# Optimization experiments

Hardware: AMD Instinct MI355X
Metric: run time of the kernel (lower is better)

Reference implementation:

```python
import jax, jax.numpy as jnp
import numpy as np


def setup_inputs() -> dict:
    key = jax.random.key(0)
    ks = jax.random.split(key, 9)
    B, L, D, H, E = 8, 2048, 1024, 256, 8
    Hg = D // 4
    s = 0.02
    return {
        "x": jax.random.normal(ks[0], (B, L, D), dtype=jnp.float32),
        "wg1": jax.random.normal(ks[1], (D, Hg), dtype=jnp.float32) * s,
        "bg1": jax.random.normal(ks[2], (Hg,), dtype=jnp.float32) * s,
        "wg2": jax.random.normal(ks[3], (Hg, E), dtype=jnp.float32) * s,
        "bg2": jax.random.normal(ks[4], (E,), dtype=jnp.float32) * s,
        "w1": jax.random.normal(ks[5], (E, D, H), dtype=jnp.float32) * (1.0 / np.sqrt(D)),
        "b1": jax.random.normal(ks[6], (E, H), dtype=jnp.float32) * s,
        "w2": jax.random.normal(ks[7], (E, H, D), dtype=jnp.float32) * (1.0 / np.sqrt(H)),
        "b2": jax.random.normal(ks[8], (E, D), dtype=jnp.float32) * s,
        "k": 2,
    }


def reference(x, wg1, bg1, wg2, bg2, w1, b1, w2, b2, k):
    B, L, D = x.shape
    xt = x.reshape(-1, D)                       # [T, D] tokens
    T = xt.shape[0]
    # gating MLP: Linear -> GELU(exact, matches torch nn.GELU) -> Linear -> softmax
    logits = jax.nn.gelu(xt @ wg1 + bg1, approximate=False) @ wg2 + bg2  # [T, E]
    scores = jax.nn.softmax(logits, axis=-1)
    top_v, top_i = jax.lax.top_k(scores, k)     # [T, k]
    # dense gate matrix (equivalent to compute_gating's scatter); zeros for non-top-k
    gates = jnp.zeros_like(scores).at[jnp.arange(T)[:, None], top_i].set(top_v)  # [T, E]

    # grouped-GEMM MoE: y[t] = sum_e gates[t,e] * (gelu(x[t] @ W1_e + b1_e) @ W2_e + b2_e)
    # scan over the fixed, small expert axis; gates zero out non-selected experts,
    # giving math identical to the sort/dispatch + per-expert torch.mm loop.
    def body(acc, we):
        w1e, b1e, w2e, b2e, ge = we
        h = jax.nn.gelu(xt @ w1e + b1e, approximate=False)  # [T, H]
        o = h @ w2e + b2e                                    # [T, D]
        return acc + ge[:, None] * o, None

    y, _ = jax.lax.scan(body, jnp.zeros_like(xt), (w1, b1, w2, b2, gates.T))
    return y.reshape(B, L, D)
```

## Files before the change

kernel.cpp:

```cpp
#include <hip/hip_runtime.h>

typedef unsigned short u16;
typedef __attribute__((ext_vector_type(8))) short bf16x8;
typedef __attribute__((ext_vector_type(4))) float f32x4;
typedef __attribute__((ext_vector_type(4))) u16 u16x4;

#define T_TOK 16384
#define D_DIM 1024
#define NE 8
#define MAXP 33792

__device__ __forceinline__ u16 f2bf(float f) {
  union { float f; unsigned int u; } c; c.f = f;
  unsigned int u = c.u;
  u += 0x7fffu + ((u >> 16) & 1u);
  return (u16)(u >> 16);
}

__device__ __forceinline__ float bf2f(u16 v) {
  union { unsigned int u; float f; } c; c.u = ((unsigned int)v) << 16;
  return c.f;
}

__device__ __forceinline__ float gelu_exact(float u) {
  return 0.5f * u * (1.0f + erff(u * 0.70710678118654752f));
}

__device__ __forceinline__ void gld16(const void* g, void* l) {
  __builtin_amdgcn_global_load_lds(
      (const __attribute__((address_space(1))) unsigned int*)g,
      (__attribute__((address_space(3))) unsigned int*)l, 16, 0, 0);
}

__device__ __forceinline__ void stage_tile(u16* lds, const char* g0, size_t stride,
                                           int wid, int lane) {
  const char* g = g0 + (size_t)(wid * 8 + (lane >> 3)) * stride + (size_t)((lane & 7) * 16);
  char* l = (char*)lds + wid * 1024;
  #pragma unroll
  for (int c = 0; c < 4; ++c)
    gld16(g + (size_t)(32 * c) * stride, l + c * 4096);
}

__device__ __forceinline__ void stage_b64x32(u16* lds, const u16* mat, int rowbase,
                                             int k0, int wid, int lane) {
  const int row = wid * 16 + (lane >> 2);
  const char* g = (const char*)(mat + (size_t)(rowbase + row) * 1024 + k0 + (lane & 3) * 8);
  char* l = (char*)lds + wid * 1024;
  gld16(g, l);
}

__device__ __forceinline__ void stage_b32(u16* lds, const u16* mat, int rowbase,
                                          int k0, int wid, int lane) {
  const char* g0 = (const char*)(mat + (size_t)rowbase * 1024 + k0);
  #pragma unroll
  for (int c = 0; c < 2; ++c) {
    const int row = c * 64 + wid * 16 + (lane >> 2);
    const char* g = g0 + (size_t)row * 2048 + (size_t)((lane & 3) * 16);
    char* l = (char*)lds + c * 4096 + wid * 1024;
    gld16(g, l);
  }
}

__device__ __forceinline__ void mma_step(const u16* As, const u16* Bs, f32x4 acc[4][4],
                                         int wm, int wn, int lane) {
  const int r = lane & 15, kq = (lane >> 4) * 8;
  #pragma unroll
  for (int ks = 0; ks < 2; ++ks) {
    const int col = ks * 32 + kq;
    bf16x8 a[4], b[4];
    #pragma unroll
    for (int mf = 0; mf < 4; ++mf)
      a[mf] = *(const bf16x8*)&As[(wm * 64 + mf * 16 + r) * 64 + col];
    #pragma unroll
    for (int nf = 0; nf < 4; ++nf)
      b[nf] = *(const bf16x8*)&Bs[(wn * 64 + nf * 16 + r) * 64 + col];
    #pragma unroll
    for (int mf = 0; mf < 4; ++mf)
      #pragma unroll
      for (int nf = 0; nf < 4; ++nf)
        acc[mf][nf] = __builtin_amdgcn_mfma_f32_16x16x32_bf16(a[mf], b[nf], acc[mf][nf], 0, 0, 0);
  }
}

__global__ __launch_bounds__(256) void cvt_hilo_x_kernel(const float* __restrict__ x,
                                                         u16* __restrict__ xh,
                                                         u16* __restrict__ xl) {
  const int i = (blockIdx.x * 256 + threadIdx.x) * 4;
  float4 v = *(const float4*)(x + i);
  float vv[4] = {v.x, v.y, v.z, v.w};
  u16x4 h, l;
  u16 hh[4], ll[4];
  #pragma unroll
  for (int q = 0; q < 4; ++q) { hh[q] = f2bf(vv[q]); ll[q] = f2bf(vv[q] - bf2f(hh[q])); }
  h.x = hh[0]; h.y = hh[1]; h.z = hh[2]; h.w = hh[3];
  l.x = ll[0]; l.y = ll[1]; l.z = ll[2]; l.w = ll[3];
  *(u16x4*)(xh + i) = h;
  *(u16x4*)(xl + i) = l;
}

__global__ __launch_bounds__(256) void transpose_cvt_kernel(const float* __restrict__ in,
                                                            u16* __restrict__ out,
                                                            int R, int C) {
  __shared__ u16 t[32][36];
  const int e = blockIdx.z;
  const int r0 = blockIdx.x * 32, c0 = blockIdx.y * 32;
  const int tid = threadIdx.x;
  {
    const int r = tid >> 3, cq = (tid & 7) * 4;
    float4 v = *(const float4*)(in + ((size_t)e * R + r0 + r) * C + c0 + cq);
    t[r][cq + 0] = f2bf(v.x); t[r][cq + 1] = f2bf(v.y);
    t[r][cq + 2] = f2bf(v.z); t[r][cq + 3] = f2bf(v.w);
  }
  __syncthreads();
  {
    const int c = tid >> 3, rq = (tid & 7) * 4;
    u16x4 o;
    o.x = t[rq + 0][c]; o.y = t[rq + 1][c]; o.z = t[rq + 2][c]; o.w = t[rq + 3][c];
    *(u16x4*)(out + ((size_t)e * C + c0 + c) * R + r0 + rq) = o;
  }
}

__global__ __launch_bounds__(256) void transpose_hilo_kernel(const float* __restrict__ in,
                                                             u16* __restrict__ out_hi,
                                                             u16* __restrict__ out_lo,
                                                             int R, int C) {
  __shared__ u16 th[32][36];
  __shared__ u16 tl[32][36];
  const int r0 = blockIdx.x * 32, c0 = blockIdx.y * 32;
  const int tid = threadIdx.x;
  {
    const int r = tid >> 3, cq = (tid & 7) * 4;
    float4 v = *(const float4*)(in + (size_t)(r0 + r) * C + c0 + cq);
    float vv[4] = {v.x, v.y, v.z, v.w};
    #pragma unroll
    for (int i = 0; i < 4; ++i) {
      u16 h = f2bf(vv[i]);
      th[r][cq + i] = h;
      tl[r][cq + i] = f2bf(vv[i] - bf2f(h));
    }
  }
  __syncthreads();
  {
    const int c = tid >> 3, rq = (tid & 7) * 4;
    u16x4 oh, ol;
    oh.x = th[rq + 0][c]; oh.y = th[rq + 1][c]; oh.z = th[rq + 2][c]; oh.w = th[rq + 3][c];
    ol.x = tl[rq + 0][c]; ol.y = tl[rq + 1][c]; ol.z = tl[rq + 2][c]; ol.w = tl[rq + 3][c];
    *(u16x4*)(out_hi + (size_t)(c0 + c) * R + r0 + rq) = oh;
    *(u16x4*)(out_lo + (size_t)(c0 + c) * R + r0 + rq) = ol;
  }
}

__global__ __launch_bounds__(256) void gating_mfma_kernel(
    const u16* __restrict__ xh, const u16* __restrict__ xl,
    const u16* __restrict__ wg1t_hi, const u16* __restrict__ wg1t_lo,
    float* __restrict__ p_buf) {
  __shared__ u16 Ah[64 * 32], Al[64 * 32];
  __shared__ u16 Bh[128 * 32], Bl[128 * 32];
  const int tid = threadIdx.x, lane = tid & 63, wid = tid >> 6;
  const int t0 = blockIdx.x * 64, n0 = blockIdx.y * 128;
  const int kh = blockIdx.z, kbeg = kh * 512;
  const int wm = wid >> 1, wn = wid & 1;

  f32x4 acc[2][4];
  #pragma unroll
  for (int i = 0; i < 2; ++i)
    #pragma unroll
    for (int j = 0; j < 4; ++j) acc[i][j] = (f32x4){0.f, 0.f, 0.f, 0.f};

  for (int kt = 0; kt < 16; ++kt) {
    const int k0 = kbeg + kt * 32;
    __syncthreads();
    stage_b64x32(Ah, xh, t0, k0, wid, lane);
    stage_b64x32(Al, xl, t0, k0, wid, lane);
    stage_b32(Bh, wg1t_hi, n0, k0, wid, lane);
    stage_b32(Bl, wg1t_lo, n0, k0, wid, lane);
    __syncthreads();
    const int r = lane & 15, ko = (lane >> 4) * 8;
    bf16x8 ah[2], al[2];
    #pragma unroll
    for (int mf = 0; mf < 2; ++mf) {
      const int ro = (wm * 32 + mf * 16 + r) * 32 + ko;
      ah[mf] = *(const bf16x8*)&Ah[ro];
      al[mf] = *(const bf16x8*)&Al[ro];
    }
    #pragma unroll
    for (int nf = 0; nf < 4; ++nf) {
      const int ro = (wn * 64 + nf * 16 + r) * 32 + ko;
      bf16x8 bh = *(const bf16x8*)&Bh[ro];
      bf16x8 bl = *(const bf16x8*)&Bl[ro];
      #pragma unroll
      for (int mf = 0; mf < 2; ++mf) {
        acc[mf][nf] = __builtin_amdgcn_mfma_f32_16x16x32_bf16(ah[mf], bh, acc[mf][nf], 0, 0, 0);
        acc[mf][nf] = __builtin_amdgcn_mfma_f32_16x16x32_bf16(ah[mf], bl, acc[mf][nf], 0, 0, 0);
        acc[mf][nf] = __builtin_amdgcn_mfma_f32_16x16x32_bf16(al[mf], bh, acc[mf][nf], 0, 0, 0);
      }
    }
  }

  #pragma unroll
  for (int mf = 0; mf < 2; ++mf)
    #pragma unroll
    for (int rr = 0; rr < 4; ++rr) {
      const int lt = wm * 32 + mf * 16 + ((lane >> 4) << 2) + rr;
      #pragma unroll
      for (int nf = 0; nf < 4; ++nf) {
        const int ln = wn * 64 + nf * 16 + (lane & 15);
        p_buf[((size_t)kh * T_TOK + t0 + lt) * 256 + n0 + ln] = acc[mf][nf][rr];
      }
    }
}

__global__ __launch_bounds__(256) void gating_p2_kernel(
    const float* __restrict__ p_buf, const float* __restrict__ bg1,
    const float* __restrict__ wg2, const float* __restrict__ bg2,
    int* __restrict__ top_i, float2* __restrict__ top_g) {
  const int tid = threadIdx.x;
  const int tn = tid & 31, tm = tid >> 5;
  const int t0 = blockIdx.x * 32;

  float bb[8];
  {
    float4 ba = *(const float4*)&bg1[tn * 4];
    float4 bc = *(const float4*)&bg1[128 + tn * 4];
    bb[0] = ba.x; bb[1] = ba.y; bb[2] = ba.z; bb[3] = ba.w;
    bb[4] = bc.x; bb[5] = bc.y; bb[6] = bc.z; bb[7] = bc.w;
  }

  float hv[4][8];
  #pragma unroll
  for (int i = 0; i < 4; ++i) {
    const size_t t = t0 + tm * 4 + i;
    const float* pa = &p_buf[t * 256];
    const float* pb = &p_buf[((size_t)T_TOK + t) * 256];
    float4 a0 = *(const float4*)&pa[tn * 4];
    float4 a1 = *(const float4*)&pa[128 + tn * 4];
    float4 b0 = *(const float4*)&pb[tn * 4];
    float4 b1 = *(const float4*)&pb[128 + tn * 4];
    hv[i][0] = gelu_exact(a0.x + b0.x + bb[0]);
    hv[i][1] = gelu_exact(a0.y + b0.y + bb[1]);
    hv[i][2] = gelu_exact(a0.z + b0.z + bb[2]);
    hv[i][3] = gelu_exact(a0.w + b0.w + bb[3]);
    hv[i][4] = gelu_exact(a1.x + b1.x + bb[4]);
    hv[i][5] = gelu_exact(a1.y + b1.y + bb[5]);
    hv[i][6] = gelu_exact(a1.z + b1.z + bb[6]);
    hv[i][7] = gelu_exact(a1.w + b1.w + bb[7]);
  }

  float part[4][8];
  #pragma unroll
  for (int i = 0; i < 4; ++i)
    #pragma unroll
    for (int e = 0; e < 8; ++e) part[i][e] = 0.f;
  #pragma unroll
  for (int j = 0; j < 8; ++j) {
    const int col = (j < 4) ? (tn * 4 + j) : (128 + tn * 4 + (j - 4));
    float4 wa = *(const float4*)&wg2[col * 8];
    float4 wb = *(const float4*)&wg2[col * 8 + 4];
    float we[8] = {wa.x, wa.y, wa.z, wa.w, wb.x, wb.y, wb.z, wb.w};
    #pragma unroll
    for (int i = 0; i < 4; ++i)
      #pragma unroll
      for (int e = 0; e < 8; ++e) part[i][e] += hv[i][j] * we[e];
  }
  #pragma unroll
  for (int mask = 1; mask < 32; mask <<= 1)
    #pragma unroll
    for (int i = 0; i < 4; ++i)
      #pragma unroll
      for (int e = 0; e < 8; ++e) part[i][e] += __shfl_xor(part[i][e], mask);

  if (tn < 4) {
    float lg[8];
    #pragma unroll
    for (int i = 0; i < 4; ++i)
      if (tn == i) {
        #pragma unroll
        for (int e = 0; e < 8; ++e) lg[e] = part[i][e];
      }
    #pragma unroll
    for (int e = 0; e < 8; ++e) lg[e] += bg2[e];
    float m = lg[0];
    #pragma unroll
    for (int e = 1; e < 8; ++e) m = fmaxf(m, lg[e]);
    float ex[8], s = 0.f;
    #pragma unroll
    for (int e = 0; e < 8; ++e) { ex[e] = expf(lg[e] - m); s += ex[e]; }
    int i1 = 0;
    #pragma unroll
    for (int e = 1; e < 8; ++e) if (lg[e] > lg[i1]) i1 = e;
    int i2 = (i1 == 0) ? 1 : 0;
    #pragma unroll
    for (int e = 0; e < 8; ++e) if (e != i1 && lg[e] > lg[i2]) i2 = e;
    float inv = 1.f / s;
    const int t = t0 + tm * 4 + tn;
    top_i[t] = i1 | (i2 << 8);
    top_g[t] = make_float2(ex[i1] * inv, ex[i2] * inv);
  }
}

__global__ __launch_bounds__(256) void hist_kernel(const int* __restrict__ top_i,
                                                   int* __restrict__ hist) {
  __shared__ int h[NE];
  const int tid = threadIdx.x;
  if (tid < NE) h[tid] = 0;
  __syncthreads();
  const int ti = top_i[blockIdx.x * 256 + tid];
  atomicAdd(&h[ti & 255], 1);
  atomicAdd(&h[ti >> 8], 1);
  __syncthreads();
  if (tid < NE) hist[blockIdx.x * NE + tid] = h[tid];
}

__global__ __launch_bounds__(64) void scan_kernel(const int* __restrict__ hist,
                                                  int* __restrict__ cnt,
                                                  int* __restrict__ offs,
                                                  int* __restrict__ cbase) {
  __shared__ int tot[NE], off_s[NE];
  const int tid = threadIdx.x;
  if (tid < NE) {
    int s = 0;
    for (int c = 0; c < 64; ++c) s += hist[c * NE + tid];
    tot[tid] = s; cnt[tid] = s;
  }
  __syncthreads();
  if (tid == 0) {
    int o = 0;
    #pragma unroll
    for (int e = 0; e < NE; ++e) { off_s[e] = o; o += (tot[e] + 127) & ~127; }
  }
  __syncthreads();
  if (tid < NE) {
    offs[tid] = off_s[tid];
    int r = off_s[tid];
    for (int c = 0; c < 64; ++c) { cbase[c * NE + tid] = r; r += hist[c * NE + tid]; }
  }
}

__global__ __launch_bounds__(256) void fill_kernel(
    const int* __restrict__ top_i, const int* __restrict__ cbase,
    int* __restrict__ tok_list, int* __restrict__ pos1, int* __restrict__ pos2) {
  __shared__ int lcnt[NE];
  const int tid = threadIdx.x;
  if (tid < NE) lcnt[tid] = 0;
  __syncthreads();
  const int t = blockIdx.x * 256 + tid;
  const int ti = top_i[t];
  const int i1 = ti & 255, i2 = ti >> 8;
  const int r1 = atomicAdd(&lcnt[i1], 1);
  const int r2 = atomicAdd(&lcnt[i2], 1);
  const int p1 = cbase[blockIdx.x * NE + i1] + r1;
  const int p2 = cbase[blockIdx.x * NE + i2] + r2;
  tok_list[p1] = t; tok_list[p2] = t;
  pos1[t] = p1; pos2[t] = p2;
}

__global__ __launch_bounds__(256) void expert_h_kernel(
    const u16* __restrict__ xb, const u16* __restrict__ w1t,
    const float* __restrict__ b1, const int* __restrict__ tok_list,
    const int* __restrict__ cnt, const int* __restrict__ offs,
    u16* __restrict__ h_c) {
  __shared__ u16 As[64 * 64];
  __shared__ u16 Bs[128 * 64];
  __shared__ float b1_s[128];
  const int e = blockIdx.z;
  const int nblk = (cnt[e] + 63) >> 6;
  if ((int)blockIdx.x >= nblk) return;
  const int tid = threadIdx.x, lane = tid & 63, wid = tid >> 6;
  const int base = offs[e] + blockIdx.x * 64;
  const int n0 = blockIdx.y * 128;
  const int wm = wid >> 1, wn = wid & 1;

  if (tid < 128) b1_s[tid] = b1[e * 256 + n0 + tid];

  int tk[2];
  #pragma unroll
  for (int c = 0; c < 2; ++c)
    tk[c] = tok_list[base + (wid * 2 + c) * 8 + (lane >> 3)];

  f32x4 acc[2][4];
  #pragma unroll
  for (int i = 0; i < 2; ++i)
    #pragma unroll
    for (int j = 0; j < 4; ++j) acc[i][j] = (f32x4){0.f, 0.f, 0.f, 0.f};

  const char* Bb = (const char*)w1t + ((size_t)e * 256 + n0) * 2048;
  const int cb = (lane & 7) * 16;
  for (int kt = 0; kt < 16; ++kt) {
    __syncthreads();
    {
      char* l = (char*)As + wid * 2048;
      #pragma unroll
      for (int c = 0; c < 2; ++c)
        gld16((const char*)xb + (size_t)tk[c] * 2048 + kt * 128 + cb, l + c * 1024);
    }
    stage_tile(Bs, Bb + kt * 128, 2048, wid, lane);
    __syncthreads();
    {
      const int r = lane & 15, kq = (lane >> 4) * 8;
      #pragma unroll
      for (int ks = 0; ks < 2; ++ks) {
        const int col = ks * 32 + kq;
        bf16x8 a[2], b[4];
        #pragma unroll
        for (int mf = 0; mf < 2; ++mf)
          a[mf] = *(const bf16x8*)&As[(wm * 32 + mf * 16 + r) * 64 + col];
        #pragma unroll
        for (int nf = 0; nf < 4; ++nf)
          b[nf] = *(const bf16x8*)&Bs[(wn * 64 + nf * 16 + r) * 64 + col];
        #pragma unroll
        for (int mf = 0; mf < 2; ++mf)
          #pragma unroll
          for (int nf = 0; nf < 4; ++nf)
            acc[mf][nf] = __builtin_amdgcn_mfma_f32_16x16x32_bf16(a[mf], b[nf], acc[mf][nf], 0, 0, 0);
      }
    }
  }

  #pragma unroll
  for (int mf = 0; mf < 2; ++mf)
    #pragma unroll
    for (int rr = 0; rr < 4; ++rr) {
      const int lt = wm * 32 + mf * 16 + ((lane >> 4) << 2) + rr;
      #pragma unroll
      for (int nf = 0; nf < 4; ++nf) {
        const int ln = wn * 64 + nf * 16 + (lane & 15);
        float u = acc[mf][nf][rr] + b1_s[ln];
        h_c[(size_t)(base + lt) * 256 + n0 + ln] = f2bf(gelu_exact(u));
      }
    }
}

__global__ __launch_bounds__(256) void moe_out_kernel(
    const u16* __restrict__ h_c, const u16* __restrict__ w2t,
    const float* __restrict__ b2, const int* __restrict__ cnt,
    const int* __restrict__ offs, u16* __restrict__ o_c) {
  __shared__ u16 As[128 * 64];
  __shared__ u16 Bs[128 * 64];
  __shared__ float b2_s[128];
  const int e = blockIdx.z;
  const int nblk = (cnt[e] + 127) >> 7;
  if ((int)blockIdx.x >= nblk) return;
  const int tid = threadIdx.x, lane = tid & 63, wid = tid >> 6;
  const int base = offs[e] + blockIdx.x * 128;
  const int n0 = blockIdx.y * 128;
  const int wm = wid >> 1, wn = wid & 1;

  if (tid < 128) b2_s[tid] = b2[(size_t)e * 1024 + n0 + tid];

  f32x4 acc[4][4];
  #pragma unroll
  for (int i = 0; i < 4; ++i)
    #pragma unroll
    for (int j = 0; j < 4; ++j) acc[i][j] = (f32x4){0.f, 0.f, 0.f, 0.f};

  const char* Ab = (const char*)h_c + (size_t)base * 512;
  const char* Bb = (const char*)w2t + ((size_t)e * D_DIM + n0) * 512;
  #pragma unroll 1
  for (int kt = 0; kt < 4; ++kt) {
    __syncthreads();
    stage_tile(As, Ab + kt * 128, 512, wid, lane);
    stage_tile(Bs, Bb + kt * 128, 512, wid, lane);
    __syncthreads();
    mma_step(As, Bs, acc, wm, wn, lane);
  }

  #pragma unroll
  for (int mf = 0; mf < 4; ++mf)
    #pragma unroll
    for (int rr = 0; rr < 4; ++rr) {
      const int lt = wm * 64 + mf * 16 + ((lane >> 4) << 2) + rr;
      #pragma unroll
      for (int nf = 0; nf < 4; ++nf) {
        const int ln = wn * 64 + nf * 16 + (lane & 15);
        o_c[(size_t)(base + lt) * 1024 + n0 + ln] = f2bf(acc[mf][nf][rr] + b2_s[ln]);
      }
    }
}

__global__ __launch_bounds__(256) void gather_kernel(
    const u16* __restrict__ o_c, const int* __restrict__ pos1,
    const int* __restrict__ pos2, const float2* __restrict__ top_g,
    float* __restrict__ y) {
  const int t = blockIdx.x;
  const int p1 = pos1[t], p2 = pos2[t];
  const float2 g = top_g[t];
  const int c = threadIdx.x * 4;
  u16x4 a = *(const u16x4*)&o_c[(size_t)p1 * 1024 + c];
  u16x4 b = *(const u16x4*)&o_c[(size_t)p2 * 1024 + c];
  float4 o;
  o.x = g.x * bf2f(a.x) + g.y * bf2f(b.x);
  o.y = g.x * bf2f(a.y) + g.y * bf2f(b.y);
  o.z = g.x * bf2f(a.z) + g.y * bf2f(b.z);
  o.w = g.x * bf2f(a.w) + g.y * bf2f(b.w);
  *(float4*)&y[(size_t)t * 1024 + c] = o;
}

extern "C" void kernel_launch(void* const* d_in, const int* in_sizes, int n_in,
                              void* d_out, int out_size, void* d_ws, size_t ws_size,
                              hipStream_t stream) {
  (void)in_sizes; (void)n_in; (void)out_size; (void)ws_size;
  const float* x   = (const float*)d_in[0];
  const float* wg1 = (const float*)d_in[1];
  const float* bg1 = (const float*)d_in[2];
  const float* wg2 = (const float*)d_in[3];
  const float* bg2 = (const float*)d_in[4];
  const float* w1  = (const float*)d_in[5];
  const float* b1  = (const float*)d_in[6];
  const float* w2  = (const float*)d_in[7];
  const float* b2  = (const float*)d_in[8];
  float* y = (float*)d_out;

  char* ws = (char*)d_ws;
  u16* xb   = (u16*)(ws);
  u16* w1t  = (u16*)(ws + 33554432);
  u16* w2t  = (u16*)(ws + 37748736);
  char* M   = ws + 41943040;
  int*    cnt      = (int*)(M);
  int*    offs     = (int*)(M + 64);
  int*    hist     = (int*)(M + 128);
  int*    cbase    = (int*)(M + 2304);
  int*    tok_list = (int*)(M + 4608);
  int*    top_i    = (int*)(M + 139776);
  float2* top_g    = (float2*)(M + 205312);
  int*    pos1     = (int*)(M + 336384);
  int*    pos2     = (int*)(M + 401920);
  u16* h_c = (u16*)(ws + 42467328);
  u16* o_c = (u16*)(ws + 59768832);
  float* p_buf   = (float*)(ws + 59768832);
  u16*   wg1t_hi = (u16*)(ws + 93323264);
  u16*   wg1t_lo = (u16*)(ws + 93847552);
  u16*   xl      = (u16*)(ws + 94371840);

  hipMemsetAsync(tok_list, 0, 135168, stream);
  cvt_hilo_x_kernel<<<16384, 256, 0, stream>>>(x, xb, xl);
  transpose_cvt_kernel<<<dim3(32, 8, 8), 256, 0, stream>>>(w1, w1t, 1024, 256);
  transpose_cvt_kernel<<<dim3(8, 32, 8), 256, 0, stream>>>(w2, w2t, 256, 1024);
  transpose_hilo_kernel<<<dim3(32, 8), 256, 0, stream>>>(wg1, wg1t_hi, wg1t_lo, 1024, 256);
  gating_mfma_kernel<<<dim3(256, 2, 2), 256, 0, stream>>>(xb, xl, wg1t_hi, wg1t_lo, p_buf);
  gating_p2_kernel<<<512, 256, 0, stream>>>(p_buf, bg1, wg2, bg2, top_i, top_g);
  hist_kernel<<<64, 256, 0, stream>>>(top_i, hist);
  scan_kernel<<<1, 64, 0, stream>>>(hist, cnt, offs, cbase);
  fill_kernel<<<64, 256, 0, stream>>>(top_i, cbase, tok_list, pos1, pos2);
  expert_h_kernel<<<dim3(256, 2, 8), 256, 0, stream>>>(xb, w1t, b1, tok_list, cnt, offs, h_c);
  moe_out_kernel <<<dim3(128, 8, 8), 256, 0, stream>>>(h_c, w2t, b2, cnt, offs, o_c);
  gather_kernel  <<<16384, 256, 0, stream>>>(o_c, pos1, pos2, top_g, y);
}
```

Baseline: 204.2 us.

## Double-buffer LDS staging in GEMM kernels and flatten expert grid over padded offsets

Adds ping-pong LDS buffers to the gating, expert_h and moe_out kernels so the global-to-LDS loads for the next K-tile are issued before the MFMA work on the current tile. This halves the barriers per iteration. The expert kernels now use a flat 1D grid of 64-row blocks over the padded token positions, finding each block's expert from the offsets, instead of a per-expert z-dimension with many early-exit blocks. moe_out shrinks from 128-row to 64-row tiles to fit the double buffers, which doubles the launched blocks and the reloading of B tiles. LDS use per block also grows, which may reduce occupancy.

```diff
diff --git a/kernel.cpp b/kernel.cpp
--- a/kernel.cpp
+++ b/kernel.cpp
@@ -39,6 +39,14 @@
   #pragma unroll
   for (int c = 0; c < 4; ++c)
     gld16(g + (size_t)(32 * c) * stride, l + c * 4096);
+}
+
+__device__ __forceinline__ void stage_a64(u16* lds, const char* g0, size_t stride,
+                                          int wid, int lane) {
+  const char* g = g0 + (size_t)(wid * 8 + (lane >> 3)) * stride + (size_t)((lane & 7) * 16);
+  char* l = (char*)lds + wid * 1024;
+  gld16(g, l);
+  gld16(g + (size_t)32 * stride, l + 4096);
 }
 
 __device__ __forceinline__ void stage_b64x32(u16* lds, const u16* mat, int rowbase,
@@ -61,25 +69,32 @@
   }
 }
 
-__device__ __forceinline__ void mma_step(const u16* As, const u16* Bs, f32x4 acc[4][4],
-                                         int wm, int wn, int lane) {
+__device__ __forceinline__ void mma_64x128(const u16* As, const u16* Bs, f32x4 acc[2][4],
+                                           int wm, int wn, int lane) {
   const int r = lane & 15, kq = (lane >> 4) * 8;
   #pragma unroll
   for (int ks = 0; ks < 2; ++ks) {
     const int col = ks * 32 + kq;
-    bf16x8 a[4], b[4];
-    #pragma unroll
-    for (int mf = 0; mf < 4; ++mf)
-      a[mf] = *(const bf16x8*)&As[(wm * 64 + mf * 16 + r) * 64 + col];
+    bf16x8 a[2], b[4];
+    #pragma unroll
+    for (int mf = 0; mf < 2; ++mf)
+      a[mf] = *(const bf16x8*)&As[(wm * 32 + mf * 16 + r) * 64 + col];
     #pragma unroll
     for (int nf = 0; nf < 4; ++nf)
       b[nf] = *(const bf16x8*)&Bs[(wn * 64 + nf * 16 + r) * 64 + col];
     #pragma unroll
-    for (int mf = 0; mf < 4; ++mf)
+    for (int mf = 0; mf < 2; ++mf)
       #pragma unroll
       for (int nf = 0; nf < 4; ++nf)
         acc[mf][nf] = __builtin_amdgcn_mfma_f32_16x16x32_bf16(a[mf], b[nf], acc[mf][nf], 0, 0, 0);
   }
+}
+
+__device__ __forceinline__ int find_expert(const int* offs, int p0) {
+  int e = 0;
+  #pragma unroll
+  for (int q = 1; q < NE; ++q) if (p0 >= offs[q]) e = q;
+  return e;
 }
 
 __global__ __launch_bounds__(256) void cvt_hilo_x_kernel(const float* __restrict__ x,
@@ -154,8 +169,8 @@
     const u16* __restrict__ xh, const u16* __restrict__ xl,
     const u16* __restrict__ wg1t_hi, const u16* __restrict__ wg1t_lo,
     float* __restrict__ p_buf) {
-  __shared__ u16 Ah[64 * 32], Al[64 * 32];
-  __shared__ u16 Bh[128 * 32], Bl[128 * 32];
+  __shared__ u16 Ah[2][64 * 32], Al[2][64 * 32];
+  __shared__ u16 Bh[2][128 * 32], Bl[2][128 * 32];
   const int tid = threadIdx.x, lane = tid & 63, wid = tid >> 6;
   const int t0 = blockIdx.x * 64, n0 = blockIdx.y * 128;
   const int kh = blockIdx.z, kbeg = kh * 512;
@@ -167,27 +182,34 @@
     #pragma unroll
     for (int j = 0; j < 4; ++j) acc[i][j] = (f32x4){0.f, 0.f, 0.f, 0.f};
 
+  stage_b64x32(Ah[0], xh, t0, kbeg, wid, lane);
+  stage_b64x32(Al[0], xl, t0, kbeg, wid, lane);
+  stage_b32(Bh[0], wg1t_hi, n0, kbeg, wid, lane);
+  stage_b32(Bl[0], wg1t_lo, n0, kbeg, wid, lane);
+  __syncthreads();
+
   for (int kt = 0; kt < 16; ++kt) {
-    const int k0 = kbeg + kt * 32;
-    __syncthreads();
-    stage_b64x32(Ah, xh, t0, k0, wid, lane);
-    stage_b64x32(Al, xl, t0, k0, wid, lane);
-    stage_b32(Bh, wg1t_hi, n0, k0, wid, lane);
-    stage_b32(Bl, wg1t_lo, n0, k0, wid, lane);
-    __syncthreads();
+    const int cur = kt & 1, nxt = cur ^ 1;
+    if (kt < 15) {
+      const int k0 = kbeg + (kt + 1) * 32;
+      stage_b64x32(Ah[nxt], xh, t0, k0, wid, lane);
+      stage_b64x32(Al[nxt], xl, t0, k0, wid, lane);
+      stage_b32(Bh[nxt], wg1t_hi, n0, k0, wid, lane);
+      stage_b32(Bl[nxt], wg1t_lo, n0, k0, wid, lane);
+    }
     const int r = lane & 15, ko = (lane >> 4) * 8;
     bf16x8 ah[2], al[2];
     #pragma unroll
     for (int mf = 0; mf < 2; ++mf) {
       const int ro = (wm * 32 + mf * 16 + r) * 32 + ko;
-      ah[mf] = *(const bf16x8*)&Ah[ro];
-      al[mf] = *(const bf16x8*)&Al[ro];
+      ah[mf] = *(const bf16x8*)&Ah[cur][ro];
+      al[mf] = *(const bf16x8*)&Al[cur][ro];
     }
     #pragma unroll
     for (int nf = 0; nf < 4; ++nf) {
       const int ro = (wn * 64 + nf * 16 + r) * 32 + ko;
-      bf16x8 bh = *(const bf16x8*)&Bh[ro];
-      bf16x8 bl = *(const bf16x8*)&Bl[ro];
+      bf16x8 bh = *(const bf16x8*)&Bh[cur][ro];
+      bf16x8 bl = *(const bf16x8*)&Bl[cur][ro];
       #pragma unroll
       for (int mf = 0; mf < 2; ++mf) {
         acc[mf][nf] = __builtin_amdgcn_mfma_f32_16x16x32_bf16(ah[mf], bh, acc[mf][nf], 0, 0, 0);
@@ -195,6 +217,7 @@
         acc[mf][nf] = __builtin_amdgcn_mfma_f32_16x16x32_bf16(al[mf], bh, acc[mf][nf], 0, 0, 0);
       }
     }
+    __syncthreads();
   }
 
   #pragma unroll
@@ -359,14 +382,13 @@
     const float* __restrict__ b1, const int* __restrict__ tok_list,
     const int* __restrict__ cnt, const int* __restrict__ offs,
     u16* __restrict__ h_c) {
-  __shared__ u16 As[64 * 64];
-  __shared__ u16 Bs[128 * 64];
+  __shared__ u16 As[2][64 * 64];
+  __shared__ u16 Bs[2][128 * 64];
   __shared__ float b1_s[128];
-  const int e = blockIdx.z;
-  const int nblk = (cnt[e] + 63) >> 6;
-  if ((int)blockIdx.x >= nblk) return;
   const int tid = threadIdx.x, lane = tid & 63, wid = tid >> 6;
-  const int base = offs[e] + blockIdx.x * 64;
+  const int base = blockIdx.x * 64;
+  const int e = find_expert(offs, base);
+  if (base >= offs[e] + ((cnt[e] + 127) & ~127)) return;
   const int n0 = blockIdx.y * 128;
   const int wm = wid >> 1, wn = wid & 1;
 
@@ -385,35 +407,27 @@
 
   const char* Bb = (const char*)w1t + ((size_t)e * 256 + n0) * 2048;
   const int cb = (lane & 7) * 16;
+
+  {
+    char* l = (char*)As[0] + wid * 2048;
+    #pragma unroll
+    for (int c = 0; c < 2; ++c)
+      gld16((const char*)xb + (size_t)tk[c] * 2048 + cb, l + c * 1024);
+    stage_tile(Bs[0], Bb, 2048, wid, lane);
+  }
+  __syncthreads();
+
   for (int kt = 0; kt < 16; ++kt) {
+    const int cur = kt & 1, nxt = cur ^ 1;
+    if (kt < 15) {
+      char* l = (char*)As[nxt] + wid * 2048;
+      #pragma unroll
+      for (int c = 0; c < 2; ++c)
+        gld16((const char*)xb + (size_t)tk[c] * 2048 + (kt + 1) * 128 + cb, l + c * 1024);
+      stage_tile(Bs[nxt], Bb + (kt + 1) * 128, 2048, wid, lane);
+    }
+    mma_64x128(As[cur], Bs[cur], acc, wm, wn, lane);
     __syncthreads();
-    {
-      char* l = (char*)As + wid * 2048;
-      #pragma unroll
-      for (int c = 0; c < 2; ++c)
-        gld16((const char*)xb + (size_t)tk[c] * 2048 + kt * 128 + cb, l + c * 1024);
-    }
-    stage_tile(Bs, Bb + kt * 128, 2048, wid, lane);
-    __syncthreads();
-    {
-      const int r = lane & 15, kq = (lane >> 4) * 8;
-      #pragma unroll
-      for (int ks = 0; ks < 2; ++ks) {
-        const int col = ks * 32 + kq;
-        bf16x8 a[2], b[4];
-        #pragma unroll
-        for (int mf = 0; mf < 2; ++mf)
-          a[mf] = *(const bf16x8*)&As[(wm * 32 + mf * 16 + r) * 64 + col];
-        #pragma unroll
-        for (int nf = 0; nf < 4; ++nf)
-          b[nf] = *(const bf16x8*)&Bs[(wn * 64 + nf * 16 + r) * 64 + col];
-        #pragma unroll
-        for (int mf = 0; mf < 2; ++mf)
-          #pragma unroll
-          for (int nf = 0; nf < 4; ++nf)
-            acc[mf][nf] = __builtin_amdgcn_mfma_f32_16x16x32_bf16(a[mf], b[nf], acc[mf][nf], 0, 0, 0);
-      }
-    }
   }
 
   #pragma unroll
@@ -434,41 +448,46 @@
     const u16* __restrict__ h_c, const u16* __restrict__ w2t,
     const float* __restrict__ b2, const int* __restrict__ cnt,
     const int* __restrict__ offs, u16* __restrict__ o_c) {
-  __shared__ u16 As[128 * 64];
-  __shared__ u16 Bs[128 * 64];
+  __shared__ u16 As[2][64 * 64];
+  __shared__ u16 Bs[2][128 * 64];
   __shared__ float b2_s[128];
-  const int e = blockIdx.z;
-  const int nblk = (cnt[e] + 127) >> 7;
-  if ((int)blockIdx.x >= nblk) return;
   const int tid = threadIdx.x, lane = tid & 63, wid = tid >> 6;
-  const int base = offs[e] + blockIdx.x * 128;
+  const int base = blockIdx.x * 64;
+  const int e = find_expert(offs, base);
+  if (base >= offs[e] + ((cnt[e] + 127) & ~127)) return;
   const int n0 = blockIdx.y * 128;
   const int wm = wid >> 1, wn = wid & 1;
 
   if (tid < 128) b2_s[tid] = b2[(size_t)e * 1024 + n0 + tid];
 
-  f32x4 acc[4][4];
-  #pragma unroll
-  for (int i = 0; i < 4; ++i)
+  f32x4 acc[2][4];
+  #pragma unroll
+  for (int i = 0; i < 2; ++i)
     #pragma unroll
     for (int j = 0; j < 4; ++j) acc[i][j] = (f32x4){0.f, 0.f, 0.f, 0.f};
 
   const char* Ab = (const char*)h_c + (size_t)base * 512;
   const char* Bb = (const char*)w2t + ((size_t)e * D_DIM + n0) * 512;
-  #pragma unroll 1
+
+  stage_a64(As[0], Ab, 512, wid, lane);
+  stage_tile(Bs[0], Bb, 512, wid, lane);
+  __syncthreads();
+
   for (int kt = 0; kt < 4; ++kt) {
+    const int cur = kt & 1, nxt = cur ^ 1;
+    if (kt < 3) {
+      stage_a64(As[nxt], Ab + (kt + 1) * 128, 512, wid, lane);
+      stage_tile(Bs[nxt], Bb + (kt + 1) * 128, 512, wid, lane);
+    }
+    mma_64x128(As[cur], Bs[cur], acc, wm, wn, lane);
     __syncthreads();
-    stage_tile(As, Ab + kt * 128, 512, wid, lane);
-    stage_tile(Bs, Bb + kt * 128, 512, wid, lane);
-    __syncthreads();
-    mma_step(As, Bs, acc, wm, wn, lane);
-  }
-
-  #pragma unroll
-  for (int mf = 0; mf < 4; ++mf)
+  }
+
+  #pragma unroll
+  for (int mf = 0; mf < 2; ++mf)
     #pragma unroll
     for (int rr = 0; rr < 4; ++rr) {
-      const int lt = wm * 64 + mf * 16 + ((lane >> 4) << 2) + rr;
+      const int lt = wm * 32 + mf * 16 + ((lane >> 4) << 2) + rr;
       #pragma unroll
       for (int nf = 0; nf < 4; ++nf) {
         const int ln = wn * 64 + nf * 16 + (lane & 15);
@@ -541,7 +560,7 @@
   hist_kernel<<<64, 256, 0, stream>>>(top_i, hist);
   scan_kernel<<<1, 64, 0, stream>>>(hist, cnt, offs, cbase);
   fill_kernel<<<64, 256, 0, stream>>>(top_i, cbase, tok_list, pos1, pos2);
-  expert_h_kernel<<<dim3(256, 2, 8), 256, 0, stream>>>(xb, w1t, b1, tok_list, cnt, offs, h_c);
-  moe_out_kernel <<<dim3(128, 8, 8), 256, 0, stream>>>(h_c, w2t, b2, cnt, offs, o_c);
+  expert_h_kernel<<<dim3(528, 2), 256, 0, stream>>>(xb, w1t, b1, tok_list, cnt, offs, h_c);
+  moe_out_kernel <<<dim3(528, 8), 256, 0, stream>>>(h_c, w2t, b2, cnt, offs, o_c);
   gather_kernel  <<<16384, 256, 0, stream>>>(o_c, pos1, pos2, top_g, y);
 }
```

New measurement: 229.2 us. 1.12x slower.
